# Optimization experiments

Measured on AMD Instinct MI355X. Metric: run time of the kernel, lower is better.

## Reference

```python
import jax, jax.numpy as jnp
import numpy as np

LOG2 = float(np.log(2.0))

def ssp(x):
    # shifted softplus: softplus(x) - softplus(0)
    return jax.nn.softplus(x) - LOG2

def layer_norm(x, g, b, eps=1e-5):
    mu = jnp.mean(x, axis=-1, keepdims=True)
    var = jnp.var(x, axis=-1, keepdims=True)
    return (x - mu) * jax.lax.rsqrt(var + eps) * g + b

def setup_inputs() -> dict:
    key = jax.random.key(0)
    ks = jax.random.split(key, 12)
    N, E, H = 100000, 600000, 128
    x = jax.random.normal(ks[0], (N, H), dtype=jnp.float32)
    edge_index = jax.random.randint(ks[1], (2, E), 0, N, dtype=jnp.int64)
    edge_attr = jax.random.normal(ks[2], (E, H), dtype=jnp.float32)
    s1 = 1.0 / np.sqrt(2 * H)
    s2 = 1.0 / np.sqrt(H)
    W1 = jax.random.uniform(ks[3], (2 * H, H), jnp.float32, -s1, s1)
    b1 = jax.random.uniform(ks[4], (H,), jnp.float32, -s1, s1)
    W2 = jax.random.uniform(ks[5], (H, H), jnp.float32, -s2, s2)
    b2 = jax.random.uniform(ks[6], (H,), jnp.float32, -s2, s2)
    W3 = jax.random.uniform(ks[7], (H, H), jnp.float32, -s2, s2)
    b3 = jax.random.uniform(ks[8], (H,), jnp.float32, -s2, s2)
    g1 = jnp.ones((H,), jnp.float32); be1 = jnp.zeros((H,), jnp.float32)
    g2 = jnp.ones((H,), jnp.float32); be2 = jnp.zeros((H,), jnp.float32)
    g3 = jnp.ones((H,), jnp.float32); be3 = jnp.zeros((H,), jnp.float32)
    return {"x": x, "edge_index": edge_index, "edge_attr": edge_attr,
            "W1": W1, "b1": b1, "g1": g1, "be1": be1,
            "W2": W2, "b2": b2, "g2": g2, "be2": be2,
            "W3": W3, "b3": b3, "g3": g3, "be3": be3}

def reference(x, edge_index, edge_attr, W1, b1, g1, be1, W2, b2, g2, be2, W3, b3, g3, be3):
    col = edge_index[1]
    # scatter_sum of edge_attr into destination nodes (segment sum)
    agg = jax.ops.segment_sum(edge_attr, col, num_segments=x.shape[0])  # [N,H]
    h = jnp.concatenate([x, agg], axis=1)  # [N,2H]
    h = ssp(layer_norm(h @ W1 + b1, g1, be1))
    h = ssp(layer_norm(h @ W2 + b2, g2, be2))
    h = ssp(layer_norm(h @ W3 + b3, g3, be3))
    return h
```

## Files before the change

### kernel.cpp

```cpp
#include <hip/hip_runtime.h>
#include <hip/hip_bf16.h>


typedef __attribute__((ext_vector_type(8))) short short8;
typedef __attribute__((ext_vector_type(4))) float f32x4;

#define NMAX 100000
#define EMAX 2000000
#define SCHUNK 2048

__device__ float g_agg[(size_t)NMAX * 128];
__device__ unsigned short g_Wp[65536];
__device__ unsigned int g_flags;
__device__ int g_hist[NMAX + 1];
__device__ int g_start[NMAX + 1];
__device__ int g_cursor[NMAX];
__device__ int g_part[1024];
__device__ int g_eid[EMAX];

__device__ inline float bf2f(unsigned int u) { return __uint_as_float(u << 16); }
__device__ inline unsigned short f2bf(float f) {
    __hip_bfloat16 h = __float2bfloat16(f);
    return *(unsigned short*)&h;
}
__device__ inline float ldp(const void* p, int i, bool bf) {
    return bf ? bf2f(((const unsigned short*)p)[i]) : ((const float*)p)[i];
}
__device__ inline float ssp_f(float x) {
    return fmaxf(x, 0.f) + log1pf(__expf(-fabsf(x))) - 0.6931471805599453f;
}

__global__ void detect_k(const unsigned int* __restrict__ g1w,
                         const unsigned int* __restrict__ eiw) {
    if (threadIdx.x == 0 && blockIdx.x == 0) {
        unsigned int f = 0;
        if (g1w[0] == 0x3F803F80u) f |= 1u;
        bool i64 = true;
        for (int i = 0; i < 8; ++i)
            if (eiw[2 * i + 1] != 0u) i64 = false;
        if (i64) f |= 2u;
        g_flags = f;
    }
}

__global__ void pack_w(const void* __restrict__ W1, const void* __restrict__ W2,
                       const void* __restrict__ W3) {
    const bool bfin = (g_flags & 1u) != 0;
    int tid = blockIdx.x * 256 + threadIdx.x;
    const void* W; int e, lg, off;
    if (tid < 32768)      { W = W1; e = tid;         lg = 3; off = 0; }
    else if (tid < 49152) { W = W2; e = tid - 32768; lg = 2; off = 32768; }
    else                  { W = W3; e = tid - 49152; lg = 2; off = 49152; }
    int j  = e & 7;
    int l  = (e >> 3) & 63;
    int kb = (e >> 9) & ((1 << lg) - 1);
    int nt = e >> (9 + lg);
    int k  = kb * 32 + ((l >> 4) * 8) + j;
    int n  = nt * 16 + (l & 15);
    float v = ldp(W, k * 128 + n, bfin);
    g_Wp[off + e] = f2bf(v);
}

__global__ void zero_hist_k(int n) {
    int i = blockIdx.x * 256 + threadIdx.x;
    if (i < n) g_hist[i] = 0;
}

__device__ inline int load_col(const void* ei, int E, int e, bool i64) {
    if (i64) return (int)((const long long*)ei)[(size_t)E + e];
    return ((const int*)ei)[E + e];
}

__global__ void hist_k(const void* __restrict__ ei, int E, int N) {
    const bool i64 = (g_flags & 2u) != 0;
    int e = blockIdx.x * 256 + threadIdx.x;
    if (e >= E) return;
    int col = load_col(ei, E, e, i64);
    if ((unsigned)col < (unsigned)N) atomicAdd(&g_hist[col], 1);
}

__global__ void scan1_k(int n) {
    __shared__ int sWave[4];
    int b = blockIdx.x, t = threadIdx.x;
    int base = b * SCHUNK + t * 8;
    int s = 0;
#pragma unroll
    for (int j = 0; j < 8; ++j) { int idx = base + j; if (idx < n) s += g_hist[idx]; }
#pragma unroll
    for (int off = 1; off < 64; off <<= 1) s += __shfl_xor(s, off);
    if ((t & 63) == 0) sWave[t >> 6] = s;
    __syncthreads();
    if (t == 0) g_part[b] = sWave[0] + sWave[1] + sWave[2] + sWave[3];
}

__global__ void scan2_k(int nb) {
    if (threadIdx.x == 0 && blockIdx.x == 0) {
        int run = 0;
        for (int i = 0; i < nb; ++i) { int v = g_part[i]; g_part[i] = run; run += v; }
    }
}

__global__ void scan3_k(int n) {
    __shared__ int sWave[4];
    int b = blockIdx.x, t = threadIdx.x;
    int base = b * SCHUNK + t * 8;
    int v[8]; int s = 0;
#pragma unroll
    for (int j = 0; j < 8; ++j) {
        int idx = base + j;
        v[j] = (idx < n) ? g_hist[idx] : 0;
        s += v[j];
    }
    int lane = t & 63, wave = t >> 6;
    int sc = s;
#pragma unroll
    for (int off = 1; off < 64; off <<= 1) {
        int o = __shfl_up(sc, off);
        if (lane >= off) sc += o;
    }
    if (lane == 63) sWave[wave] = sc;
    __syncthreads();
    int woff = 0;
#pragma unroll
    for (int w = 0; w < 4; ++w) if (w < wave) woff += sWave[w];
    int excl = sc - s + woff + g_part[b];
#pragma unroll
    for (int j = 0; j < 8; ++j) {
        int idx = base + j;
        if (idx < n) { g_start[idx] = excl; if (idx < n - 1) g_cursor[idx] = excl; }
        excl += v[j];
    }
}

__global__ void scatter_ids_k(const void* __restrict__ ei, int E, int N) {
    const bool i64 = (g_flags & 2u) != 0;
    int e = blockIdx.x * 256 + threadIdx.x;
    if (e >= E) return;
    int col = load_col(ei, E, e, i64);
    if ((unsigned)col >= (unsigned)N) return;
    int pos = atomicAdd(&g_cursor[col], 1);
    if (pos < EMAX) g_eid[pos] = e;
}

__global__ void __launch_bounds__(256) agg_k(const void* __restrict__ ea, int N) {
    const bool bfin = (g_flags & 1u) != 0;
    int wv = (blockIdx.x * 256 + threadIdx.x) >> 6;
    int lane = threadIdx.x & 63;
    if (wv >= N) return;
    int s = g_start[wv], e = g_start[wv + 1];
    float ax = 0.f, ay = 0.f;
    if (bfin) {
        int i = s;
        for (; i + 1 < e; i += 2) {
            int e0 = g_eid[i], e1 = g_eid[i + 1];
            unsigned int u0 = *(const unsigned int*)((const unsigned short*)ea + (size_t)e0 * 128 + lane * 2);
            unsigned int u1 = *(const unsigned int*)((const unsigned short*)ea + (size_t)e1 * 128 + lane * 2);
            ax += bf2f(u0 & 0xffffu) + bf2f(u1 & 0xffffu);
            ay += bf2f(u0 >> 16)     + bf2f(u1 >> 16);
        }
        if (i < e) {
            unsigned int u0 = *(const unsigned int*)((const unsigned short*)ea + (size_t)g_eid[i] * 128 + lane * 2);
            ax += bf2f(u0 & 0xffffu);
            ay += bf2f(u0 >> 16);
        }
    } else {
        int i = s;
        for (; i + 1 < e; i += 2) {
            int e0 = g_eid[i], e1 = g_eid[i + 1];
            float2 v0 = *(const float2*)((const float*)ea + (size_t)e0 * 128 + lane * 2);
            float2 v1 = *(const float2*)((const float*)ea + (size_t)e1 * 128 + lane * 2);
            ax += v0.x + v1.x;
            ay += v0.y + v1.y;
        }
        if (i < e) {
            float2 v0 = *(const float2*)((const float*)ea + (size_t)g_eid[i] * 128 + lane * 2);
            ax += v0.x;
            ay += v0.y;
        }
    }
    float2 o; o.x = ax; o.y = ay;
    *(float2*)(g_agg + (size_t)wv * 128 + lane * 2) = o;
}

template <int KBCNT>
__device__ inline void mfma_stage(const unsigned short* __restrict__ sAb, int strideA,
                                  const unsigned short* __restrict__ Wp,
                                  const void* __restrict__ bias, bool bfin,
                                  float* __restrict__ sH, int lane, int wave) {
    const int mt = wave & 1, nh = wave >> 1;
    const int mrow = mt * 16 + (lane & 15);
    const int koff = (lane >> 4) * 8;
    short8 af[KBCNT];
#pragma unroll
    for (int kb = 0; kb < KBCNT; ++kb)
        af[kb] = *(const short8*)(sAb + mrow * strideA + kb * 32 + koff);
#pragma unroll
    for (int i = 0; i < 4; ++i) {
        int nt = nh * 4 + i;
        f32x4 acc = {0.f, 0.f, 0.f, 0.f};
        const unsigned short* wp = Wp + ((size_t)(nt * KBCNT) * 64 + lane) * 8;
#pragma unroll
        for (int kb = 0; kb < KBCNT; ++kb) {
            short8 bf = *(const short8*)(wp + kb * 512);
            acc = __builtin_amdgcn_mfma_f32_16x16x32_bf16(af[kb], bf, acc, 0, 0, 0);
        }
        int col = nt * 16 + (lane & 15);
        float bv = ldp(bias, col, bfin);
        int rbase = mt * 16 + (lane >> 4) * 4;
#pragma unroll
        for (int r = 0; r < 4; ++r)
            sH[(rbase + r) * 132 + col] = acc[r] + bv;
    }
}

template <bool TOGLOBAL>
__device__ inline void ln_stage(const float* __restrict__ sH, void* dstv, int strideD,
                                const void* __restrict__ g, const void* __restrict__ be,
                                int t, int validRows, bool bfin, bool bfout) {
    int row = t >> 3, seg = t & 7;
    const float* hp = sH + row * 132 + seg * 16;
    float v[16];
    float s = 0.f, ss = 0.f;
#pragma unroll
    for (int j = 0; j < 16; ++j) { float x = hp[j]; v[j] = x; s += x; ss += x * x; }
    s += __shfl_xor(s, 1);  ss += __shfl_xor(ss, 1);
    s += __shfl_xor(s, 2);  ss += __shfl_xor(ss, 2);
    s += __shfl_xor(s, 4);  ss += __shfl_xor(ss, 4);
    float mu  = s * (1.f / 128.f);
    float var = ss * (1.f / 128.f) - mu * mu;
    float rs  = rsqrtf(var + 1e-5f);
    float y[16];
#pragma unroll
    for (int j = 0; j < 16; ++j) {
        int fidx = seg * 16 + j;
        y[j] = ssp_f((v[j] - mu) * rs * ldp(g, fidx, bfin) + ldp(be, fidx, bfin));
    }
    if (TOGLOBAL && row >= validRows) return;
    if (!TOGLOBAL || bfout) {
        alignas(16) unsigned short o[16];
#pragma unroll
        for (int j = 0; j < 16; ++j) o[j] = f2bf(y[j]);
        unsigned short* d = (unsigned short*)dstv + row * strideD + seg * 16;
        *(uint4*)(d)     = ((const uint4*)o)[0];
        *(uint4*)(d + 8) = ((const uint4*)o)[1];
    } else {
        float* d = (float*)dstv + row * strideD + seg * 16;
#pragma unroll
        for (int j = 0; j < 4; ++j)
            ((float4*)d)[j] = ((const float4*)y)[j];
    }
}

__global__ void __launch_bounds__(256)
mlp_fused(const void* __restrict__ x,
          const void* b1, const void* g1, const void* be1,
          const void* b2, const void* g2, const void* be2,
          const void* b3, const void* g3, const void* be3,
          void* __restrict__ out, int N) {
    __shared__ alignas(16) unsigned short sA[32 * 264];
    __shared__ alignas(16) float sH[32 * 132];
    __shared__ alignas(16) unsigned short sA2[32 * 136];
    const unsigned int fl = g_flags;
    const bool bfin = (fl & 1u) != 0;
    const bool bfout = bfin;
    const int t = threadIdx.x, lane = t & 63, wave = t >> 6;
    const long node0 = (long)blockIdx.x * 32;
    const int validRows = (int)min((long)32, (long)N - node0);

    for (int i = t; i < 512; i += 256) {
        int r = i >> 4, c = (i & 15) * 8;
        long node = node0 + r; if (node >= N) node = N - 1;
        if (bfin) {
            *(short8*)(sA + r * 264 + c) =
                *(const short8*)((const unsigned short*)x + node * 128 + c);
        } else {
            const float* p = (const float*)x + node * 128 + c;
            float4 a = *(const float4*)p, b = *(const float4*)(p + 4);
            alignas(16) unsigned short o[8] = {f2bf(a.x),f2bf(a.y),f2bf(a.z),f2bf(a.w),
                                               f2bf(b.x),f2bf(b.y),f2bf(b.z),f2bf(b.w)};
            *(uint4*)(sA + r * 264 + c) = *(const uint4*)o;
        }
    }
    for (int i = t; i < 512; i += 256) {
        int r = i >> 4, c = (i & 15) * 8;
        long node = node0 + r; if (node >= N) node = N - 1;
        const float* p = g_agg + (size_t)node * 128 + c;
        float4 a = *(const float4*)p, b = *(const float4*)(p + 4);
        alignas(16) unsigned short o[8] = {f2bf(a.x),f2bf(a.y),f2bf(a.z),f2bf(a.w),
                                           f2bf(b.x),f2bf(b.y),f2bf(b.z),f2bf(b.w)};
        *(uint4*)(sA + r * 264 + 128 + c) = *(const uint4*)o;
    }
    __syncthreads();

    mfma_stage<8>(sA, 264, g_Wp, b1, bfin, sH, lane, wave);
    __syncthreads();
    ln_stage<false>(sH, sA2, 136, g1, be1, t, 32, bfin, true);
    __syncthreads();
    mfma_stage<4>(sA2, 136, g_Wp + 32768, b2, bfin, sH, lane, wave);
    __syncthreads();
    ln_stage<false>(sH, sA, 136, g2, be2, t, 32, bfin, true);
    __syncthreads();
    mfma_stage<4>(sA, 136, g_Wp + 49152, b3, bfin, sH, lane, wave);
    __syncthreads();
    if (bfout)
        ln_stage<true>(sH, (unsigned short*)out + node0 * 128, 128, g3, be3, t, validRows, bfin, true);
    else
        ln_stage<true>(sH, (float*)out + node0 * 128, 128, g3, be3, t, validRows, bfin, false);
}

extern "C" void kernel_launch(void* const* d_in, const int* in_sizes, int n_in,
                              void* d_out, int out_size, void* d_ws, size_t ws_size,
                              hipStream_t stream) {
    const void* x   = d_in[0];
    const void* ei  = d_in[1];
    const void* ea  = d_in[2];
    const void* W1  = d_in[3];
    const void* b1  = d_in[4];
    const void* g1  = d_in[5];
    const void* be1 = d_in[6];
    const void* W2  = d_in[7];
    const void* b2  = d_in[8];
    const void* g2  = d_in[9];
    const void* be2 = d_in[10];
    const void* W3  = d_in[11];
    const void* b3  = d_in[12];
    const void* g3  = d_in[13];
    const void* be3 = d_in[14];

    int N = in_sizes[0] / 128;
    if (N > NMAX) N = NMAX;
    int E = in_sizes[2] / 128;
    if (E > EMAX) E = EMAX;

    detect_k<<<1, 64, 0, stream>>>((const unsigned int*)g1, (const unsigned int*)ei);
    pack_w<<<256, 256, 0, stream>>>(W1, W2, W3);

    int nh = N + 1;
    zero_hist_k<<<(nh + 255) / 256, 256, 0, stream>>>(nh);
    hist_k<<<(E + 255) / 256, 256, 0, stream>>>(ei, E, N);
    int nb = (nh + SCHUNK - 1) / SCHUNK;
    scan1_k<<<nb, 256, 0, stream>>>(nh);
    scan2_k<<<1, 64, 0, stream>>>(nb);
    scan3_k<<<nb, 256, 0, stream>>>(nh);
    scatter_ids_k<<<(E + 255) / 256, 256, 0, stream>>>(ei, E, N);

    agg_k<<<(N + 3) / 4, 256, 0, stream>>>(ea, N);

    mlp_fused<<<(N + 31) / 32, 256, 0, stream>>>(x, b1, g1, be1, b2, g2, be2, b3, g3, be3,
                                                 d_out, N);
}
```

Before: 740.5 us.

## Fuse edge aggregation into MLP kernel and merge init kernels

```diff
diff --git a/kernel.cpp b/kernel.cpp
--- a/kernel.cpp
+++ b/kernel.cpp
@@ -9,7 +9,6 @@
 #define EMAX 2000000
 #define SCHUNK 2048
 
-__device__ float g_agg[(size_t)NMAX * 128];
 __device__ unsigned short g_Wp[65536];
 __device__ unsigned int g_flags;
 __device__ int g_hist[NMAX + 1];
@@ -27,17 +26,37 @@
     return bf ? bf2f(((const unsigned short*)p)[i]) : ((const float*)p)[i];
 }
 __device__ inline float ssp_f(float x) {
-    return fmaxf(x, 0.f) + log1pf(__expf(-fabsf(x))) - 0.6931471805599453f;
-}
-
-__global__ void detect_k(const unsigned int* __restrict__ g1w,
-                         const unsigned int* __restrict__ eiw) {
-    if (threadIdx.x == 0 && blockIdx.x == 0) {
+    float t = __expf(-fabsf(x));
+    return fmaxf(x, 0.f) + __logf(1.f + t) - 0.6931471805599453f;
+}
+
+__device__ inline void load16(const void* p, int off, bool bf, float* out) {
+    if (bf) {
+        const unsigned short* q = (const unsigned short*)p + off;
+        uint4 u0 = *(const uint4*)q, u1 = *(const uint4*)(q + 8);
+        unsigned int w[8] = {u0.x, u0.y, u0.z, u0.w, u1.x, u1.y, u1.z, u1.w};
+#pragma unroll
+        for (int j = 0; j < 8; ++j) {
+            out[2 * j]     = bf2f(w[j] & 0xffffu);
+            out[2 * j + 1] = bf2f(w[j] >> 16);
+        }
+    } else {
+        const float* q = (const float*)p + off;
+#pragma unroll
+        for (int j = 0; j < 4; ++j) ((float4*)out)[j] = ((const float4*)q)[j];
+    }
+}
+
+__global__ void init_k(const unsigned int* __restrict__ g1w,
+                       const unsigned int* __restrict__ eiw, int nh) {
+    int i = blockIdx.x * 256 + threadIdx.x;
+    if (i < nh) g_hist[i] = 0;
+    if (i == 0) {
         unsigned int f = 0;
         if (g1w[0] == 0x3F803F80u) f |= 1u;
         bool i64 = true;
-        for (int i = 0; i < 8; ++i)
-            if (eiw[2 * i + 1] != 0u) i64 = false;
+        for (int k = 0; k < 8; ++k)
+            if (eiw[2 * k + 1] != 0u) i64 = false;
         if (i64) f |= 2u;
         g_flags = f;
     }
@@ -61,11 +80,6 @@
     g_Wp[off + e] = f2bf(v);
 }
 
-__global__ void zero_hist_k(int n) {
-    int i = blockIdx.x * 256 + threadIdx.x;
-    if (i < n) g_hist[i] = 0;
-}
-
 __device__ inline int load_col(const void* ei, int E, int e, bool i64) {
     if (i64) return (int)((const long long*)ei)[(size_t)E + e];
     return ((const int*)ei)[E + e];
@@ -139,47 +153,7 @@
     int col = load_col(ei, E, e, i64);
     if ((unsigned)col >= (unsigned)N) return;
     int pos = atomicAdd(&g_cursor[col], 1);
-    if (pos < EMAX) g_eid[pos] = e;
-}
-
-__global__ void __launch_bounds__(256) agg_k(const void* __restrict__ ea, int N) {
-    const bool bfin = (g_flags & 1u) != 0;
-    int wv = (blockIdx.x * 256 + threadIdx.x) >> 6;
-    int lane = threadIdx.x & 63;
-    if (wv >= N) return;
-    int s = g_start[wv], e = g_start[wv + 1];
-    float ax = 0.f, ay = 0.f;
-    if (bfin) {
-        int i = s;
-        for (; i + 1 < e; i += 2) {
-            int e0 = g_eid[i], e1 = g_eid[i + 1];
-            unsigned int u0 = *(const unsigned int*)((const unsigned short*)ea + (size_t)e0 * 128 + lane * 2);
-            unsigned int u1 = *(const unsigned int*)((const unsigned short*)ea + (size_t)e1 * 128 + lane * 2);
-            ax += bf2f(u0 & 0xffffu) + bf2f(u1 & 0xffffu);
-            ay += bf2f(u0 >> 16)     + bf2f(u1 >> 16);
-        }
-        if (i < e) {
-            unsigned int u0 = *(const unsigned int*)((const unsigned short*)ea + (size_t)g_eid[i] * 128 + lane * 2);
-            ax += bf2f(u0 & 0xffffu);
-            ay += bf2f(u0 >> 16);
-        }
-    } else {
-        int i = s;
-        for (; i + 1 < e; i += 2) {
-            int e0 = g_eid[i], e1 = g_eid[i + 1];
-            float2 v0 = *(const float2*)((const float*)ea + (size_t)e0 * 128 + lane * 2);
-            float2 v1 = *(const float2*)((const float*)ea + (size_t)e1 * 128 + lane * 2);
-            ax += v0.x + v1.x;
-            ay += v0.y + v1.y;
-        }
-        if (i < e) {
-            float2 v0 = *(const float2*)((const float*)ea + (size_t)g_eid[i] * 128 + lane * 2);
-            ax += v0.x;
-            ay += v0.y;
-        }
-    }
-    float2 o; o.x = ax; o.y = ay;
-    *(float2*)(g_agg + (size_t)wv * 128 + lane * 2) = o;
+    if (pos >= 0 && pos < EMAX) g_eid[pos] = e;
 }
 
 template <int KBCNT>
@@ -222,19 +196,22 @@
     float v[16];
     float s = 0.f, ss = 0.f;
 #pragma unroll
-    for (int j = 0; j < 16; ++j) { float x = hp[j]; v[j] = x; s += x; ss += x * x; }
+    for (int j = 0; j < 4; ++j) ((float4*)v)[j] = ((const float4*)hp)[j];
+#pragma unroll
+    for (int j = 0; j < 16; ++j) { float x = v[j]; s += x; ss += x * x; }
     s += __shfl_xor(s, 1);  ss += __shfl_xor(ss, 1);
     s += __shfl_xor(s, 2);  ss += __shfl_xor(ss, 2);
     s += __shfl_xor(s, 4);  ss += __shfl_xor(ss, 4);
     float mu  = s * (1.f / 128.f);
     float var = ss * (1.f / 128.f) - mu * mu;
     float rs  = rsqrtf(var + 1e-5f);
+    float gv[16], bv[16];
+    load16(g,  seg * 16, bfin, gv);
+    load16(be, seg * 16, bfin, bv);
     float y[16];
 #pragma unroll
-    for (int j = 0; j < 16; ++j) {
-        int fidx = seg * 16 + j;
-        y[j] = ssp_f((v[j] - mu) * rs * ldp(g, fidx, bfin) + ldp(be, fidx, bfin));
-    }
+    for (int j = 0; j < 16; ++j)
+        y[j] = ssp_f((v[j] - mu) * rs * gv[j] + bv[j]);
     if (TOGLOBAL && row >= validRows) return;
     if (!TOGLOBAL || bfout) {
         alignas(16) unsigned short o[16];
@@ -252,7 +229,7 @@
 }
 
 __global__ void __launch_bounds__(256)
-mlp_fused(const void* __restrict__ x,
+mlp_fused(const void* __restrict__ x, const void* __restrict__ ea,
           const void* b1, const void* g1, const void* be1,
           const void* b2, const void* g2, const void* be2,
           const void* b3, const void* g3, const void* be3,
@@ -281,14 +258,74 @@
             *(uint4*)(sA + r * 264 + c) = *(const uint4*)o;
         }
     }
-    for (int i = t; i < 512; i += 256) {
-        int r = i >> 4, c = (i & 15) * 8;
-        long node = node0 + r; if (node >= N) node = N - 1;
-        const float* p = g_agg + (size_t)node * 128 + c;
-        float4 a = *(const float4*)p, b = *(const float4*)(p + 4);
-        alignas(16) unsigned short o[8] = {f2bf(a.x),f2bf(a.y),f2bf(a.z),f2bf(a.w),
-                                           f2bf(b.x),f2bf(b.y),f2bf(b.z),f2bf(b.w)};
-        *(uint4*)(sA + r * 264 + 128 + c) = *(const uint4*)o;
+
+    {
+        int row = t >> 3, seg = t & 7;
+        long node = node0 + row; if (node >= N) node = N - 1;
+        int s0 = g_start[node], e2 = g_start[node + 1];
+        if (s0 < 0) s0 = 0;
+        if (e2 > EMAX) e2 = EMAX;
+        float acc[16];
+#pragma unroll
+        for (int j = 0; j < 16; ++j) acc[j] = 0.f;
+        if (bfin) {
+            int i = s0;
+            for (; i + 1 < e2; i += 2) {
+                const unsigned short* p0 = (const unsigned short*)ea + (size_t)g_eid[i] * 128 + seg * 16;
+                const unsigned short* p1 = (const unsigned short*)ea + (size_t)g_eid[i + 1] * 128 + seg * 16;
+                uint4 u0 = *(const uint4*)p0, u1 = *(const uint4*)(p0 + 8);
+                uint4 v0 = *(const uint4*)p1, v1 = *(const uint4*)(p1 + 8);
+                unsigned int w0[8] = {u0.x,u0.y,u0.z,u0.w,u1.x,u1.y,u1.z,u1.w};
+                unsigned int w1[8] = {v0.x,v0.y,v0.z,v0.w,v1.x,v1.y,v1.z,v1.w};
+#pragma unroll
+                for (int j = 0; j < 8; ++j) {
+                    acc[2*j]   += bf2f(w0[j] & 0xffffu) + bf2f(w1[j] & 0xffffu);
+                    acc[2*j+1] += bf2f(w0[j] >> 16)     + bf2f(w1[j] >> 16);
+                }
+            }
+            if (i < e2) {
+                const unsigned short* p0 = (const unsigned short*)ea + (size_t)g_eid[i] * 128 + seg * 16;
+                uint4 u0 = *(const uint4*)p0, u1 = *(const uint4*)(p0 + 8);
+                unsigned int w0[8] = {u0.x,u0.y,u0.z,u0.w,u1.x,u1.y,u1.z,u1.w};
+#pragma unroll
+                for (int j = 0; j < 8; ++j) {
+                    acc[2*j]   += bf2f(w0[j] & 0xffffu);
+                    acc[2*j+1] += bf2f(w0[j] >> 16);
+                }
+            }
+        } else {
+            int i = s0;
+            for (; i + 1 < e2; i += 2) {
+                const float* p0 = (const float*)ea + (size_t)g_eid[i] * 128 + seg * 16;
+                const float* p1 = (const float*)ea + (size_t)g_eid[i + 1] * 128 + seg * 16;
+#pragma unroll
+                for (int j = 0; j < 4; ++j) {
+                    float4 a = ((const float4*)p0)[j];
+                    float4 b = ((const float4*)p1)[j];
+                    acc[4*j]   += a.x + b.x;
+                    acc[4*j+1] += a.y + b.y;
+                    acc[4*j+2] += a.z + b.z;
+                    acc[4*j+3] += a.w + b.w;
+                }
+            }
+            if (i < e2) {
+                const float* p0 = (const float*)ea + (size_t)g_eid[i] * 128 + seg * 16;
+#pragma unroll
+                for (int j = 0; j < 4; ++j) {
+                    float4 a = ((const float4*)p0)[j];
+                    acc[4*j]   += a.x;
+                    acc[4*j+1] += a.y;
+                    acc[4*j+2] += a.z;
+                    acc[4*j+3] += a.w;
+                }
+            }
+        }
+        alignas(16) unsigned short o[16];
+#pragma unroll
+        for (int j = 0; j < 16; ++j) o[j] = f2bf(acc[j]);
+        unsigned short* d = sA + row * 264 + 128 + seg * 16;
+        *(uint4*)(d)     = ((const uint4*)o)[0];
+        *(uint4*)(d + 8) = ((const uint4*)o)[1];
     }
     __syncthreads();
 
@@ -332,11 +369,11 @@
     int E = in_sizes[2] / 128;
     if (E > EMAX) E = EMAX;
 
-    detect_k<<<1, 64, 0, stream>>>((const unsigned int*)g1, (const unsigned int*)ei);
+    int nh = N + 1;
+    init_k<<<(nh + 255) / 256, 256, 0, stream>>>((const unsigned int*)g1,
+                                                 (const unsigned int*)ei, nh);
     pack_w<<<256, 256, 0, stream>>>(W1, W2, W3);
 
-    int nh = N + 1;
-    zero_hist_k<<<(nh + 255) / 256, 256, 0, stream>>>(nh);
     hist_k<<<(E + 255) / 256, 256, 0, stream>>>(ei, E, N);
     int nb = (nh + SCHUNK - 1) / SCHUNK;
     scan1_k<<<nb, 256, 0, stream>>>(nh);
@@ -344,8 +381,6 @@
     scan3_k<<<nb, 256, 0, stream>>>(nh);
     scatter_ids_k<<<(E + 255) / 256, 256, 0, stream>>>(ei, E, N);
 
-    agg_k<<<(N + 3) / 4, 256, 0, stream>>>(ea, N);
-
-    mlp_fused<<<(N + 31) / 32, 256, 0, stream>>>(x, b1, g1, be1, b2, g2, be2, b3, g3, be3,
-                                                 d_out, N);
-}
+    mlp_fused<<<(N + 31) / 32, 256, 0, stream>>>(x, ea, b1, g1, be1, b2, g2, be2,
+                                                 b3, g3, be3, d_out, N);
+}
```

Measured after the change: 610.7 us. 17.5% less time.
